# Performance work log

Hardware: AMD Instinct MI355X
Metric: run time of the kernel (lower is better)

The kernel has to match this reference:

```python
import jax, jax.numpy as jnp
import numpy as np

N, HID, MAXD, B, NCLS, GRUH = 50000, 128, 16, 50, 10, 32


def setup_inputs() -> dict:
    key = jax.random.key(0)
    ks = jax.random.split(key, 18)
    s = 0.05
    nrm = lambda k, shp: (jax.random.normal(k, shp, jnp.float32) * s)
    return {
        "feature": jax.random.normal(ks[0], (N, HID), jnp.float32),
        "nbr_idx": jax.random.randint(ks[1], (N, MAXD), 0, N, dtype=jnp.int32),
        "deg": jax.random.randint(ks[2], (N,), 1, MAXD + 1, dtype=jnp.int32),
        "graph_ids": (jnp.arange(N, dtype=jnp.int32) * B) // N,
        # SAGEConv(lstm) params: LSTM(in=HID, hidden=HID) + fc_self/fc_neigh
        "lstm_Wih": nrm(ks[3], (4 * HID, HID)),
        "lstm_Whh": nrm(ks[4], (4 * HID, HID)),
        "lstm_bih": nrm(ks[5], (4 * HID,)),
        "lstm_bhh": nrm(ks[6], (4 * HID,)),
        "W_self": nrm(ks[7], (HID, HID)),
        "W_neigh": nrm(ks[8], (HID, HID)),
        "b_sage": nrm(ks[9], (HID,)),
        # GraphConv params
        "W_gc": nrm(ks[10], (HID, HID)),
        "b_gc": nrm(ks[11], (HID,)),
        # GRU params (h0=0 so weight_hh contributes nothing; only its bias matters)
        "Wih_gru": nrm(ks[12], (3 * GRUH, HID)),
        "bih_gru": nrm(ks[13], (3 * GRUH,)),
        "bhh_gru": nrm(ks[14], (3 * GRUH,)),
        # classifier (dropout is identity at eval)
        "W_cls": nrm(ks[15], (GRUH, NCLS)),
        "b_cls": nrm(ks[16], (NCLS,)),
    }


def _lstm_aggregate(feats, nbr_idx, deg, Wih, Whh, bih, bhh):
    # DGL SAGEConv 'lstm' reducer: run LSTM over each node's neighbor features,
    # take final hidden state. Implemented as a masked scan over padded lists.
    n, hdim = feats.shape
    h0 = jnp.zeros((n, hdim), feats.dtype)

    def step(carry, t):
        h, c = carry
        x = feats[jnp.take(nbr_idx, t, axis=1)]  # [N, HID] gather of t-th neighbor
        gates = x @ Wih.T + bih + h @ Whh.T + bhh
        i, f, g, o = jnp.split(gates, 4, axis=-1)  # torch gate order i,f,g,o
        c_new = jax.nn.sigmoid(f) * c + jax.nn.sigmoid(i) * jnp.tanh(g)
        h_new = jax.nn.sigmoid(o) * jnp.tanh(c_new)
        valid = (t < deg)[:, None]
        return (jnp.where(valid, h_new, h), jnp.where(valid, c_new, c)), None

    (hT, _), _ = jax.lax.scan(step, (h0, h0), jnp.arange(nbr_idx.shape[1]))
    return hT  # hidden at each node's last valid neighbor


def _graph_conv(h, nbr_idx, deg, W, b):
    # DGL GraphConv norm='both': D^-1/2 A D^-1/2 h W + b
    n, maxd = nbr_idx.shape
    norm = jax.lax.rsqrt(jnp.maximum(deg.astype(h.dtype), 1.0))
    hn = h * norm[:, None]
    mask = (jnp.arange(maxd, dtype=jnp.int32)[None, :] < deg[:, None]).astype(h.dtype)
    contrib = hn[nbr_idx.reshape(-1)] * mask.reshape(-1)[:, None]  # [N*MAXD, HID]
    dst = jnp.repeat(jnp.arange(n, dtype=jnp.int32), maxd)
    agg = jax.ops.segment_sum(contrib, dst, num_segments=n)
    return (agg * norm[:, None]) @ W + b


def _gru_step(x, Wih, bih, bhh):
    # single GRU step with h0 = 0 (seq_len == 1 in the original view(1, N, H))
    gh = x @ Wih.T + bih  # [N, 3*GRUH]
    xr, xz, xn = jnp.split(gh, 3, axis=-1)  # torch gate order r,z,n
    br, bz, bn = jnp.split(bhh, 3)
    r = jax.nn.sigmoid(xr + br)
    z = jax.nn.sigmoid(xz + bz)
    nst = jnp.tanh(xn + r * bn)
    return (1.0 - z) * nst  # h' = (1-z)*n + z*h0, h0 = 0


def reference(feature, nbr_idx, deg, graph_ids, lstm_Wih, lstm_Whh, lstm_bih,
              lstm_bhh, W_self, W_neigh, b_sage, W_gc, b_gc, Wih_gru, bih_gru,
              bhh_gru, W_cls, b_cls):
    # conv4: SAGEConv lstm -> relu
    h_nei = _lstm_aggregate(feature, nbr_idx, deg, lstm_Wih, lstm_Whh, lstm_bih, lstm_bhh)
    h = jax.nn.relu(feature @ W_self + h_nei @ W_neigh + b_sage)
    # conv2: GraphConv -> relu
    h = jax.nn.relu(_graph_conv(h, nbr_idx, deg, W_gc, b_gc))
    # GRU over seq_len=1, batch=N
    out = _gru_step(h, Wih_gru, bih_gru, bhh_gru)  # [N, 32]
    # dgl.mean_nodes: per-graph mean pool
    sums = jax.ops.segment_sum(out, graph_ids, num_segments=B)
    cnts = jax.ops.segment_sum(jnp.ones((out.shape[0],), out.dtype), graph_ids, num_segments=B)
    hg = sums / cnts[:, None]
    # classify (Dropout is identity in eval)
    return hg @ W_cls + b_cls  # [B, NCLS]
```

## Files before the change

kernel.cpp:

```cpp
#include <hip/hip_runtime.h>
#include <hip/hip_bf16.h>


#define NN     50000
#define HIDD   128
#define MAXD   16
#define NGRAPH 50
#define NCLSS  10
#define GRUH   32

typedef __attribute__((ext_vector_type(8))) short s16x8;
typedef __attribute__((ext_vector_type(4))) float f32x4;
typedef __hip_bfloat16 bf16;

#define MFMA16(a,b,c)  __builtin_amdgcn_mfma_f32_16x16x32_bf16((a),(b),(c),0,0,0)

__device__ __forceinline__ float bf2f(bf16 x) { return __bfloat162float(x); }
__device__ __forceinline__ bf16  f2bf(float x) { return __float2bfloat16(x); }
__device__ __forceinline__ s16x8 ldfrag(const bf16* p) { return *(const s16x8*)p; }

__device__ __forceinline__ s16x8 ldfrag_f32(const float* p) {
  const float4 a = *(const float4*)p;
  const float4 b = *(const float4*)(p + 4);
  union { s16x8 v; bf16 h[8]; } r;
  r.h[0] = f2bf(a.x); r.h[1] = f2bf(a.y); r.h[2] = f2bf(a.z); r.h[3] = f2bf(a.w);
  r.h[4] = f2bf(b.x); r.h[5] = f2bf(b.y); r.h[6] = f2bf(b.z); r.h[7] = f2bf(b.w);
  return r.v;
}

__device__ __forceinline__ float sigf(float x) {
  return __builtin_amdgcn_rcpf(1.0f + __expf(-x));
}
__device__ __forceinline__ float tanhf_(float x) {
  return 1.0f - 2.0f * __builtin_amdgcn_rcpf(1.0f + __expf(2.0f * x));
}

__device__ __forceinline__ unsigned packbf2(float a, float b) {
  union { bf16 h; unsigned short u; } x, y;
  x.h = f2bf(a); y.h = f2bf(b);
  return (unsigned)x.u | ((unsigned)y.u << 16);
}
__device__ __forceinline__ float lo2f(unsigned u) { return __uint_as_float(u << 16); }
__device__ __forceinline__ float hi2f(unsigned u) { return __uint_as_float(u & 0xffff0000u); }

__device__ __forceinline__ void lgkm_barrier() {
  asm volatile("s_waitcnt lgkmcnt(0)\n\ts_barrier" ::: "memory");
}

__global__ __launch_bounds__(256) void prep_kernel(const float* __restrict__ Wih,
                            const float* __restrict__ Whh, const float* __restrict__ bih,
                            const float* __restrict__ bhh, const float* __restrict__ Wself,
                            const float* __restrict__ Wneigh, const float* __restrict__ Wgc,
                            const float* __restrict__ Wgru, const int* __restrict__ deg,
                            bf16* WihB, bf16* WhhB, bf16* WsT, bf16* WnT,
                            bf16* WgT, bf16* WgruB, float* biasS,
                            int* histp, int* resv, float* psums, int* done) {
  __shared__ int lh[17];
  const int tid = threadIdx.x;
  const bool histblk = (blockIdx.x < 196);
  if (histblk) {
    if (tid < 17) lh[tid] = 0;
    __syncthreads();
    const int i = blockIdx.x * 256 + tid;
    if (i < NN) atomicAdd(&lh[deg[i]], 1);
    __syncthreads();
    if (tid < 17) histp[blockIdx.x * 17 + tid] = lh[tid];
  }
  if (blockIdx.x == 0) {
    for (int i = tid; i < 17; i += 256) resv[i] = 0;
    for (int i = tid; i < NGRAPH * GRUH + NGRAPH; i += 256) psums[i] = 0.f;
    if (tid == 0) *done = 0;
  }
  const int total = 2 * 65536 + 3 * 16384 + 12288 + 512;
  int stride = gridDim.x * blockDim.x;
  for (int idx = blockIdx.x * blockDim.x + threadIdx.x; idx < total; idx += stride) {
    int j = idx;
    if (j < 65536) { WihB[j] = f2bf(Wih[j]); continue; }
    j -= 65536;
    if (j < 65536) { WhhB[j] = f2bf(Whh[j]); continue; }
    j -= 65536;
    if (j < 16384) { int c = j >> 7, k = j & 127; WsT[j] = f2bf(Wself[k * HIDD + c]); continue; }
    j -= 16384;
    if (j < 16384) { int c = j >> 7, k = j & 127; WnT[j] = f2bf(Wneigh[k * HIDD + c]); continue; }
    j -= 16384;
    if (j < 16384) { int c = j >> 7, k = j & 127; WgT[j] = f2bf(Wgc[k * HIDD + c]); continue; }
    j -= 16384;
    if (j < 12288) { WgruB[j] = f2bf(Wgru[j]); continue; }
    j -= 12288;
    biasS[j] = bih[j] + bhh[j];
  }
}

__global__ __launch_bounds__(256) void sg_kernel(const float* __restrict__ featF,
                                                 const bf16* __restrict__ WihB,
                                                 const float* __restrict__ biasS,
                                                 bf16* __restrict__ Gp,
                                                 const int* __restrict__ deg,
                                                 const int* __restrict__ histp,
                                                 int* __restrict__ resv,
                                                 int* __restrict__ perm) {
  const int tid = threadIdx.x;
  if (blockIdx.x >= 782) {
    __shared__ int lh[17], lbase[17], lpos[17], gh[17];
    const int sb = blockIdx.x - 782;
    if (tid < 17) { lh[tid] = 0; lpos[tid] = 0; }
    __syncthreads();
    const int i = sb * 256 + tid;
    const int d = (i < NN) ? deg[i] : -1;
    if (d >= 0) atomicAdd(&lh[d], 1);
    __syncthreads();
    if (tid < 17) {
      int s = 0;
      for (int b = 0; b < 196; ++b) s += histp[b * 17 + tid];
      gh[tid] = s;
    }
    __syncthreads();
    if (tid < 17) {
      int pre = 0;
      for (int k = tid + 1; k < 17; ++k) pre += gh[k];
      lbase[tid] = pre + (lh[tid] ? atomicAdd(&resv[tid], lh[tid]) : 0);
    }
    __syncthreads();
    if (d >= 0) {
      const int p = lbase[d] + atomicAdd(&lpos[d], 1);
      perm[p] = i;
    }
    return;
  }
  __shared__ __align__(16) bf16 Gs[32][520];
  const int lane = tid & 63, wave = tid >> 6;
  const int l15 = lane & 15, quad = lane >> 4;
  const int nb = blockIdx.x * 64;

  s16x8 Bx[4][4];
#pragma unroll
  for (int nt = 0; nt < 4; ++nt) {
    int arow = nb + nt * 16 + l15; if (arow >= NN) arow = NN - 1;
#pragma unroll
    for (int kt = 0; kt < 4; ++kt)
      Bx[nt][kt] = ldfrag_f32(featF + (size_t)arow * HIDD + kt * 32 + quad * 8);
  }

#pragma unroll
  for (int pass = 0; pass < 2; ++pass) {
    for (int hg = wave * 8; hg < wave * 8 + 8; ++hg) {
      const int wr = (l15 & 3) * HIDD + hg * 4 + (l15 >> 2);
      s16x8 Aw[4];
#pragma unroll
      for (int kt = 0; kt < 4; ++kt)
        Aw[kt] = ldfrag(WihB + (size_t)wr * HIDD + kt * 32 + quad * 8);
      const int hcol = hg * 4 + quad;
      const int gbase = (hcol >> 3) * 32 + (hcol & 3) * 8 + ((hcol >> 2) & 1) * 4;
      float b0 = biasS[0 * HIDD + hcol], b1 = biasS[1 * HIDD + hcol];
      float b2 = biasS[2 * HIDD + hcol], b3 = biasS[3 * HIDD + hcol];
#pragma unroll
      for (int nt2 = 0; nt2 < 2; ++nt2) {
        const int nt = pass * 2 + nt2;
        f32x4 acc = {0.f, 0.f, 0.f, 0.f};
#pragma unroll
        for (int kt = 0; kt < 4; ++kt)
          acc = MFMA16(Aw[kt], Bx[nt][kt], acc);
        unsigned u0 = packbf2(acc[0] + b0, acc[1] + b1);
        unsigned u1 = packbf2(acc[2] + b2, acc[3] + b3);
        *(uint2*)(&Gs[nt2 * 16 + l15][gbase]) = make_uint2(u0, u1);
      }
    }
    __syncthreads();
    for (int e = tid; e < 2048; e += 256) {
      const int r = e >> 6, off = (e & 63) * 8;
      const int node = nb + pass * 32 + r;
      if (node < NN)
        *(s16x8*)(Gp + (size_t)node * 512 + off) = *(const s16x8*)(&Gs[r][off]);
    }
    __syncthreads();
  }
}

__global__ __launch_bounds__(1024, 4) void lstm_kernel(const bf16* __restrict__ Gp,
                                                       const bf16* __restrict__ WhhB,
                                                       const float* __restrict__ featF,
                                                       const bf16* __restrict__ WsT,
                                                       const bf16* __restrict__ WnT,
                                                       const float* __restrict__ b_sage,
                                                       const int* __restrict__ nbr_idx,
                                                       const int* __restrict__ deg,
                                                       const int* __restrict__ perm,
                                                       bf16* __restrict__ h1n) {
  __shared__ __align__(16) bf16 Hs[2][64 * 128];
  __shared__ int nbr_s[16 * 64];
  __shared__ int nodes_s[64];
  __shared__ int degs_s[64];

  const int tid = threadIdx.x;
  const int lane = tid & 63, w = tid >> 6;
  const int l15 = lane & 15, quad = lane >> 4;
  const int base = blockIdx.x * 64;

  if (tid < 64) {
    const int gi = base + tid;
    const int nd = (gi < NN) ? perm[gi] : -1;
    nodes_s[tid] = nd;
    degs_s[tid] = (nd >= 0) ? deg[nd] : 0;
  }
  __syncthreads();
  {
    const int row = tid & 63, t = tid >> 6;
    const int nd = nodes_s[row];
    nbr_s[t * 64 + row] = (nd >= 0) ? nbr_idx[nd * MAXD + t] : 0;
  }

  s16x8 Bh[2][4];
#pragma unroll
  for (int gt = 0; gt < 2; ++gt) {
    const int wr = (l15 & 3) * HIDD + w * 8 + gt * 4 + (l15 >> 2);
#pragma unroll
    for (int kt = 0; kt < 4; ++kt) {
      Bh[gt][kt] = ldfrag(WhhB + (size_t)wr * HIDD + kt * 32 + quad * 8);
      asm volatile("" : "+v"(Bh[gt][kt]));
    }
  }

  __syncthreads();
  const int maxdeg = degs_s[0];

  int mydeg[4];
#pragma unroll
  for (int nt = 0; nt < 4; ++nt) mydeg[nt] = degs_s[nt * 16 + l15];

  const int gofs = w * 32 + quad * 8;

  float cst[2][4] = {{0.f, 0.f, 0.f, 0.f}, {0.f, 0.f, 0.f, 0.f}};
  float hprev[2][4] = {{0.f, 0.f, 0.f, 0.f}, {0.f, 0.f, 0.f, 0.f}};

  for (int t = 0; t < maxdeg; ++t) {
    const int cur = t & 1, nxt = cur ^ 1;

    uint2 gx[2][4];
#pragma unroll
    for (int nt = 0; nt < 4; ++nt) {
      const int nb1 = nbr_s[t * 64 + nt * 16 + l15];
      const uint4 g4 = *(const uint4*)(Gp + (size_t)nb1 * 512 + gofs);
      gx[0][nt] = make_uint2(g4.x, g4.y);
      gx[1][nt] = make_uint2(g4.z, g4.w);
    }

    f32x4 acc[2][4];
#pragma unroll
    for (int gt = 0; gt < 2; ++gt)
#pragma unroll
      for (int nt = 0; nt < 4; ++nt) acc[gt][nt] = (f32x4){0.f, 0.f, 0.f, 0.f};

    if (t > 0) {
      __builtin_amdgcn_s_setprio(1);
#pragma unroll
      for (int kt = 0; kt < 4; ++kt) {
#pragma unroll
        for (int nt = 0; nt < 4; ++nt) {
          const int row = nt * 16 + l15;
          const s16x8 ah = ldfrag(Hs[cur] + row * 128 + (((kt * 4 + quad) ^ l15) * 8));
#pragma unroll
          for (int gt = 0; gt < 2; ++gt)
            acc[gt][nt] = MFMA16(Bh[gt][kt], ah, acc[gt][nt]);
        }
      }
      __builtin_amdgcn_s_setprio(0);
    }

#pragma unroll
    for (int gt = 0; gt < 2; ++gt) {
      const int col = w * 8 + gt * 4 + quad;
#pragma unroll
      for (int nt = 0; nt < 4; ++nt) {
        const int row = nt * 16 + l15;
        const uint2 g = gx[gt][nt];
        const float g_i = acc[gt][nt][0] + lo2f(g.x);
        const float g_f = acc[gt][nt][1] + hi2f(g.x);
        const float g_g = acc[gt][nt][2] + lo2f(g.y);
        const float g_o = acc[gt][nt][3] + hi2f(g.y);
        const float iv = sigf(g_i), fv = sigf(g_f);
        const float gv = tanhf_(g_g), ov = sigf(g_o);
        const float cn = fv * cst[gt][nt] + iv * gv;
        const float hn_new = ov * tanhf_(cn);
        const bool act = (t < mydeg[nt]);
        if (act) cst[gt][nt] = cn;
        const float hn = act ? hn_new : hprev[gt][nt];
        hprev[gt][nt] = hn;
        Hs[nxt][row * 128 + ((w ^ (row & 15)) * 8) + (col & 7)] = f2bf(hn);
      }
    }
    lgkm_barrier();
  }

  const bf16* Hf = Hs[maxdeg & 1];
  {
    const int rq = w & 3, cp = w >> 2;
    const int rowA = rq * 16 + l15;
    const int ndA = nodes_s[rowA];
    const int ndA2 = (ndA >= 0) ? ndA : 0;
    s16x8 Fa[4], Ha[4];
#pragma unroll
    for (int kt = 0; kt < 4; ++kt) {
      Fa[kt] = ldfrag_f32(featF + (size_t)ndA2 * HIDD + kt * 32 + quad * 8);
      Ha[kt] = ldfrag(Hf + rowA * 128 + (((kt * 4 + quad) ^ l15) * 8));
    }
    int ndC[4]; float nrmC[4];
#pragma unroll
    for (int r = 0; r < 4; ++r) {
      const int rowC = rq * 16 + quad * 4 + r;
      ndC[r] = nodes_s[rowC];
      const int dd = degs_s[rowC];
      nrmC[r] = rsqrtf((float)((dd > 0) ? dd : 1));
    }
#pragma unroll
    for (int cc = 0; cc < 2; ++cc) {
      const int col = (cp * 2 + cc) * 16 + l15;
      f32x4 acc = {0.f, 0.f, 0.f, 0.f};
#pragma unroll
      for (int kt = 0; kt < 4; ++kt) {
        acc = MFMA16(Fa[kt], ldfrag(WsT + col * HIDD + kt * 32 + quad * 8), acc);
        acc = MFMA16(Ha[kt], ldfrag(WnT + col * HIDD + kt * 32 + quad * 8), acc);
      }
      const float bb = b_sage[col];
#pragma unroll
      for (int r = 0; r < 4; ++r)
        if (ndC[r] >= 0)
          h1n[(size_t)ndC[r] * HIDD + col] = f2bf(fmaxf(acc[r] + bb, 0.f) * nrmC[r]);
    }
  }
}

__global__ __launch_bounds__(256) void aggru_kernel(const bf16* __restrict__ h1n,
                                                    const int* __restrict__ nbr_idx,
                                                    const int* __restrict__ deg,
                                                    const int* __restrict__ gids,
                                                    const bf16* __restrict__ WgT,
                                                    const float* __restrict__ b_gc,
                                                    const bf16* __restrict__ WgruB,
                                                    const float* __restrict__ bih,
                                                    const float* __restrict__ bhh,
                                                    float* __restrict__ psums,
                                                    float* __restrict__ pcnts,
                                                    int* __restrict__ done,
                                                    const float* __restrict__ Wcls,
                                                    const float* __restrict__ bcls,
                                                    float* __restrict__ out) {
  __shared__ __align__(16) bf16 Ag[64 * 136];
  __shared__ __align__(16) bf16 H2[64 * 136];
  __shared__ int nbrL[64 * 16];
  __shared__ float psl[2 * GRUH];
  __shared__ float pcl[2];
  __shared__ int ticket_s;
  const int tid = threadIdx.x;
  const int lane = tid & 63, wave = tid >> 6;
  const int l15 = lane & 15, quad = lane >> 4;
  const int nbb = blockIdx.x * 64;
  const int nb = nbb + wave * 16;

  if (tid < 2 * GRUH) psl[tid] = 0.f;
  if (tid < 2) pcl[tid] = 0.f;

  for (int e = tid; e < 64 * 16; e += 256) {
    const int node = nbb + (e >> 4);
    nbrL[e] = (node < NN) ? nbr_idx[node * MAXD + (e & 15)] : 0;
  }
  __syncthreads();

  {
    const int myn = tid >> 2;
    const int node = nbb + myn;
    const int seg = (tid & 3) * 32;
    const int d = (node < NN) ? deg[node] : 0;
    float accv[32];
#pragma unroll
    for (int k = 0; k < 32; ++k) accv[k] = 0.f;
#pragma unroll 2
    for (int j = 0; j < d; ++j) {
      const int nbr = nbrL[myn * 16 + j];
      const bf16* rp = h1n + (size_t)nbr * HIDD + seg;
#pragma unroll
      for (int f = 0; f < 4; ++f) {
        union { s16x8 v; unsigned u[4]; } t_;
        t_.v = ldfrag(rp + f * 8);
#pragma unroll
        for (int p = 0; p < 4; ++p) {
          accv[f * 8 + 2 * p]     += lo2f(t_.u[p]);
          accv[f * 8 + 2 * p + 1] += hi2f(t_.u[p]);
        }
      }
    }
    const float nm = (d > 0) ? rsqrtf((float)d) : 0.f;
#pragma unroll
    for (int f = 0; f < 4; ++f) {
      union { s16x8 v; bf16 h[8]; } o;
#pragma unroll
      for (int k = 0; k < 8; ++k) o.h[k] = f2bf(accv[f * 8 + k] * nm);
      *(s16x8*)(Ag + myn * 136 + seg + f * 8) = o.v;
    }
  }
  __syncthreads();

  s16x8 A[4];
#pragma unroll
  for (int kt = 0; kt < 4; ++kt)
    A[kt] = ldfrag(Ag + (wave * 16 + l15) * 136 + kt * 32 + quad * 8);
  for (int ct = 0; ct < 8; ++ct) {
    const int col = ct * 16 + l15;
    f32x4 acc = {0.f, 0.f, 0.f, 0.f};
#pragma unroll
    for (int kt = 0; kt < 4; ++kt)
      acc = MFMA16(A[kt], ldfrag(WgT + col * HIDD + kt * 32 + quad * 8), acc);
    const float bb = b_gc[col];
#pragma unroll
    for (int r = 0; r < 4; ++r)
      H2[(wave * 16 + quad * 4 + r) * 136 + col] = f2bf(fmaxf(acc[r] + bb, 0.f));
  }
  __syncthreads();

  s16x8 A2[4];
#pragma unroll
  for (int kt = 0; kt < 4; ++kt)
    A2[kt] = ldfrag(H2 + (wave * 16 + l15) * 136 + kt * 32 + quad * 8);
  f32x4 acc[6];
#pragma unroll
  for (int ct = 0; ct < 6; ++ct) {
    f32x4 a = {0.f, 0.f, 0.f, 0.f};
#pragma unroll
    for (int kt = 0; kt < 4; ++kt)
      a = MFMA16(A2[kt], ldfrag(WgruB + (ct * 16 + l15) * HIDD + kt * 32 + quad * 8), a);
    acc[ct] = a;
  }

  const int g0 = gids[nbb];
  int mynode[4], mygs[4];
#pragma unroll
  for (int r = 0; r < 4; ++r) {
    const int nd = nb + quad * 4 + r;
    mynode[r] = nd;
    mygs[r] = (nd < NN) ? (gids[nd] - g0) : 0;
  }
#pragma unroll
  for (int u = 0; u < 2; ++u) {
    const int cu = 16 * u + l15;
    const float br = bih[cu] + bhh[cu];
    const float bz = bih[32 + cu] + bhh[32 + cu];
    const float bni = bih[64 + cu];
    const float bnh = bhh[64 + cu];
#pragma unroll
    for (int r = 0; r < 4; ++r) {
      if (mynode[r] < NN) {
        const float rv = sigf(acc[u][r] + br);
        const float zv = sigf(acc[2 + u][r] + bz);
        const float nv = tanhf_(acc[4 + u][r] + bni + rv * bnh);
        const float v = (1.f - zv) * nv;
        atomicAdd(&psl[mygs[r] * GRUH + cu], v);
        if (u == 0 && l15 == 0) atomicAdd(&pcl[mygs[r]], 1.f);
      }
    }
  }
  __syncthreads();
  if (tid < 2 * GRUH) {
    const int s = tid >> 5, c = tid & 31;
    const float vv = psl[tid];
    if (vv != 0.f && g0 + s < NGRAPH) atomicAdd(&psums[(g0 + s) * GRUH + c], vv);
  }
  if (tid < 2) {
    if (pcl[tid] != 0.f && g0 + tid < NGRAPH) atomicAdd(&pcnts[g0 + tid], pcl[tid]);
  }

  __threadfence();
  if (tid == 0) ticket_s = atomicAdd(done, 1);
  __syncthreads();
  if (ticket_s == (int)gridDim.x - 1) {
    __shared__ float ps[NGRAPH * GRUH];
    __shared__ float pc[NGRAPH];
    for (int i = tid; i < NGRAPH * GRUH; i += 256) ps[i] = atomicAdd(&psums[i], 0.f);
    for (int i = tid; i < NGRAPH; i += 256) pc[i] = atomicAdd(&pcnts[i], 0.f);
    __syncthreads();
    for (int idx = tid; idx < NGRAPH * NCLSS; idx += 256) {
      const int g = idx / NCLSS, k = idx % NCLSS;
      const float inv = 1.0f / pc[g];
      float accо = bcls[k];
#pragma unroll
      for (int cc = 0; cc < GRUH; ++cc)
        accо += ps[g * GRUH + cc] * inv * Wcls[cc * NCLSS + k];
      out[idx] = accо;
    }
  }
}

extern "C" void kernel_launch(void* const* d_in, const int* in_sizes, int n_in,
                              void* d_out, int out_size, void* d_ws, size_t ws_size,
                              hipStream_t stream) {
  const float* feature  = (const float*)d_in[0];
  const int*   nbr_idx  = (const int*)d_in[1];
  const int*   deg      = (const int*)d_in[2];
  const int*   gids     = (const int*)d_in[3];
  const float* lstm_Wih = (const float*)d_in[4];
  const float* lstm_Whh = (const float*)d_in[5];
  const float* lstm_bih = (const float*)d_in[6];
  const float* lstm_bhh = (const float*)d_in[7];
  const float* W_self   = (const float*)d_in[8];
  const float* W_neigh  = (const float*)d_in[9];
  const float* b_sage   = (const float*)d_in[10];
  const float* W_gc     = (const float*)d_in[11];
  const float* b_gc     = (const float*)d_in[12];
  const float* Wih_gru  = (const float*)d_in[13];
  const float* bih_gru  = (const float*)d_in[14];
  const float* bhh_gru  = (const float*)d_in[15];
  const float* W_cls    = (const float*)d_in[16];
  const float* b_cls    = (const float*)d_in[17];

  char* ws = (char*)d_ws;
  bf16*  h1nB  = (bf16*)(ws + 0);
  bf16*  Gp    = (bf16*)(ws + 12800000);
  const size_t wo = 64000000;
  bf16*  WihB  = (bf16*)(ws + wo);
  bf16*  WhhB  = (bf16*)(ws + wo + 131072);
  bf16*  WsT   = (bf16*)(ws + wo + 262144);
  bf16*  WnT   = (bf16*)(ws + wo + 294912);
  bf16*  WgT   = (bf16*)(ws + wo + 327680);
  bf16*  WgruB = (bf16*)(ws + wo + 360448);
  float* biasS = (float*)(ws + wo + 385024);
  int*   perm  = (int*)(ws + 64500000);
  int*   histp = (int*)(ws + 64800000);
  int*   resv  = (int*)(ws + 64814000);
  float* psums = (float*)(ws + 64815000);
  float* pcnts = (float*)(ws + 64821400);
  int*   done  = (int*)(ws + 64821600);

  prep_kernel<<<754, 256, 0, stream>>>(lstm_Wih, lstm_Whh, lstm_bih, lstm_bhh,
                                       W_self, W_neigh, W_gc, Wih_gru, deg,
                                       WihB, WhhB, WsT, WnT, WgT, WgruB, biasS,
                                       histp, resv, psums, done);
  sg_kernel<<<978, 256, 0, stream>>>(feature, WihB, biasS, Gp, deg, histp, resv, perm);
  lstm_kernel<<<782, 1024, 0, stream>>>(Gp, WhhB, feature, WsT, WnT, b_sage,
                                        nbr_idx, deg, perm, h1nB);
  aggru_kernel<<<782, 256, 0, stream>>>(h1nB, nbr_idx, deg, gids, WgT, b_gc,
                                        WgruB, bih_gru, bhh_gru, psums, pcnts,
                                        done, W_cls, b_cls, (float*)d_out);
}
```

Baseline: 407.8 us.

## Fuse LSTM gate math into fewer exp/rcp ops and pack hidden-state writes

Rewrites the LSTM cell update so the sigmoid and tanh gates share one combined reciprocal, using a few exps and two rcp instructions instead of separate sigmoid/tanh calls. It also remaps the gate-column layout of the Wih-preprojected gates and the Whh fragment rows so each lane holds two adjacent hidden columns. This lets the new hidden state go to shared memory as one packed bf16x2 store instead of two scalar stores. The final reduction reuses existing shared buffers instead of declaring new shared arrays, and replaces the threadfence with a vmcnt wait on one thread. The factored expression may lose accuracy or overflow for large gate magnitudes, and the weaker fence may have ordering risks.

```diff
diff --git a/kernel.cpp b/kernel.cpp
--- a/kernel.cpp
+++ b/kernel.cpp
@@ -57,8 +57,7 @@
                             int* histp, int* resv, float* psums, int* done) {
   __shared__ int lh[17];
   const int tid = threadIdx.x;
-  const bool histblk = (blockIdx.x < 196);
-  if (histblk) {
+  if (blockIdx.x < 196) {
     if (tid < 17) lh[tid] = 0;
     __syncthreads();
     const int i = blockIdx.x * 256 + tid;
@@ -150,7 +149,7 @@
       for (int kt = 0; kt < 4; ++kt)
         Aw[kt] = ldfrag(WihB + (size_t)wr * HIDD + kt * 32 + quad * 8);
       const int hcol = hg * 4 + quad;
-      const int gbase = (hcol >> 3) * 32 + (hcol & 3) * 8 + ((hcol >> 2) & 1) * 4;
+      const int gbase = (hcol >> 3) * 32 + ((hcol >> 1) & 3) * 8 + (hcol & 1) * 4;
       float b0 = biasS[0 * HIDD + hcol], b1 = biasS[1 * HIDD + hcol];
       float b2 = biasS[2 * HIDD + hcol], b3 = biasS[3 * HIDD + hcol];
 #pragma unroll
@@ -212,7 +211,7 @@
   s16x8 Bh[2][4];
 #pragma unroll
   for (int gt = 0; gt < 2; ++gt) {
-    const int wr = (l15 & 3) * HIDD + w * 8 + gt * 4 + (l15 >> 2);
+    const int wr = (l15 & 3) * HIDD + w * 8 + (l15 >> 2) * 2 + gt;
 #pragma unroll
     for (int kt = 0; kt < 4; ++kt) {
       Bh[gt][kt] = ldfrag(WhhB + (size_t)wr * HIDD + kt * 32 + quad * 8);
@@ -267,26 +266,35 @@
     }
 
 #pragma unroll
-    for (int gt = 0; gt < 2; ++gt) {
-      const int col = w * 8 + gt * 4 + quad;
-#pragma unroll
-      for (int nt = 0; nt < 4; ++nt) {
-        const int row = nt * 16 + l15;
+    for (int nt = 0; nt < 4; ++nt) {
+      const int row = nt * 16 + l15;
+      const bool act = (t < mydeg[nt]);
+      float hnv[2];
+#pragma unroll
+      for (int gt = 0; gt < 2; ++gt) {
         const uint2 g = gx[gt][nt];
         const float g_i = acc[gt][nt][0] + lo2f(g.x);
         const float g_f = acc[gt][nt][1] + hi2f(g.x);
         const float g_g = acc[gt][nt][2] + lo2f(g.y);
         const float g_o = acc[gt][nt][3] + hi2f(g.y);
-        const float iv = sigf(g_i), fv = sigf(g_f);
-        const float gv = tanhf_(g_g), ov = sigf(g_o);
-        const float cn = fv * cst[gt][nt] + iv * gv;
-        const float hn_new = ov * tanhf_(cn);
-        const bool act = (t < mydeg[nt]);
+        const float Ae = __expf(-g_i);
+        const float Fe = __expf(-g_f);
+        const float Be = __expf(-2.f * g_g);
+        const float Ce = __expf(-g_o);
+        const float Qf = 1.f + Fe;
+        const float P  = (1.f + Ae) * (1.f + Be);
+        const float num = cst[gt][nt] * P + (1.f - Be) * Qf;
+        const float cn = num * __builtin_amdgcn_rcpf(Qf * P);
+        const float De = __expf(-2.f * cn);
+        const float hn_new =
+            (1.f - De) * __builtin_amdgcn_rcpf((1.f + Ce) * (1.f + De));
         if (act) cst[gt][nt] = cn;
         const float hn = act ? hn_new : hprev[gt][nt];
         hprev[gt][nt] = hn;
-        Hs[nxt][row * 128 + ((w ^ (row & 15)) * 8) + (col & 7)] = f2bf(hn);
+        hnv[gt] = hn;
       }
+      *(unsigned*)(&Hs[nxt][row * 128 + ((w ^ (row & 15)) * 8) + quad * 2]) =
+          packbf2(hnv[0], hnv[1]);
     }
     lgkm_barrier();
   }
@@ -467,23 +475,25 @@
     if (pcl[tid] != 0.f && g0 + tid < NGRAPH) atomicAdd(&pcnts[g0 + tid], pcl[tid]);
   }
 
-  __threadfence();
-  if (tid == 0) ticket_s = atomicAdd(done, 1);
+  if (tid == 0) {
+    asm volatile("s_waitcnt vmcnt(0)" ::: "memory");
+    ticket_s = atomicAdd(done, 1);
+  }
   __syncthreads();
   if (ticket_s == (int)gridDim.x - 1) {
-    __shared__ float ps[NGRAPH * GRUH];
-    __shared__ float pc[NGRAPH];
+    float* ps = (float*)Ag;
+    float* pc = (float*)H2;
     for (int i = tid; i < NGRAPH * GRUH; i += 256) ps[i] = atomicAdd(&psums[i], 0.f);
     for (int i = tid; i < NGRAPH; i += 256) pc[i] = atomicAdd(&pcnts[i], 0.f);
     __syncthreads();
     for (int idx = tid; idx < NGRAPH * NCLSS; idx += 256) {
       const int g = idx / NCLSS, k = idx % NCLSS;
       const float inv = 1.0f / pc[g];
-      float accо = bcls[k];
+      float a = bcls[k];
 #pragma unroll
       for (int cc = 0; cc < GRUH; ++cc)
-        accо += ps[g * GRUH + cc] * inv * Wcls[cc * NCLSS + k];
-      out[idx] = accо;
+        a += ps[g * GRUH + cc] * inv * Wcls[cc * NCLSS + k];
+      out[idx] = a;
     }
   }
 }
```

Measured after the change: 375.6 us. 7.9% less time.
